# Optimization experiments

Hardware: AMD Instinct MI355X
Metric: run time of the kernel (lower is better)

Reference implementation:

```python
import jax, jax.numpy as jnp
import numpy as np

K = 31  # AvgPool2d kernel size
P = 15  # padding


def _box_avg(x):
    """31x31 stride-1 avg pool, count_include_pad=True (PyTorch default):
    separable ones-conv with zero padding, divided by K*K."""
    B, C, H, W = x.shape
    kh = jnp.ones((C, 1, K, 1), x.dtype)
    kw = jnp.ones((C, 1, 1, K), x.dtype)
    dn = ('NCHW', 'OIHW', 'NCHW')
    y = jax.lax.conv_general_dilated(x, kh, (1, 1), [(P, P), (0, 0)],
                                     dimension_numbers=dn, feature_group_count=C)
    y = jax.lax.conv_general_dilated(y, kw, (1, 1), [(0, 0), (P, P)],
                                     dimension_numbers=dn, feature_group_count=C)
    return y / (K * K)


def setup_inputs() -> dict:
    key = jax.random.key(0)
    k1, k2 = jax.random.split(key)
    pred = jax.random.normal(k1, (64, 1, 512, 512), dtype=jnp.float32)
    mask = jax.random.uniform(k2, (64, 1, 512, 512), dtype=jnp.float32)
    return {"pred": pred, "mask": mask}


def reference(pred, mask):
    weit = 1.0 + 5.0 * jnp.abs(_box_avg(mask) - mask)
    p = jax.nn.sigmoid(pred)
    inter = jnp.sum(p * mask * weit, axis=(2, 3))          # [B, C]
    union = jnp.sum((p + mask) * weit, axis=(2, 3))        # [B, C]
    wdiss = 1.0 - (2.0 * inter + 0.5) / (union + 0.5)
    return jnp.mean(wdiss)
```

## Files before the change

kernel.cpp:

```cpp
#include <hip/hip_runtime.h>
#include <math.h>

#define NB 64
#define HH 512
#define WW 512
#define KK 31
#define PP 15
#define TS 32
#define NSTRIP (HH / TS)
#define HR (TS + KK - 1)
#define NPAIR (HR / 2)

typedef _Float16 f16;
typedef f16 f16x8 __attribute__((ext_vector_type(8)));
typedef f16 f16x4 __attribute__((ext_vector_type(4)));
typedef f16 f16x2 __attribute__((ext_vector_type(2)));

__device__ __forceinline__ f16x2 shfl_up2(f16x2 v, int delta) {
    int x = __shfl_up(__builtin_bit_cast(int, v), delta);
    return __builtin_bit_cast(f16x2, x);
}
__device__ __forceinline__ f16x2 shfl_dn2(f16x2 v, int delta) {
    int x = __shfl_down(__builtin_bit_cast(int, v), delta);
    return __builtin_bit_cast(f16x2, x);
}
__device__ __forceinline__ f16x2 sel2(bool c, f16x2 v) {
    f16x2 z = {(f16)0, (f16)0};
    return c ? v : z;
}
__device__ __forceinline__ void keep4(float4& v) {
    asm volatile("" : "+v"(v.x), "+v"(v.y), "+v"(v.z), "+v"(v.w));
}


__global__ __launch_bounds__(512, 4) void dice_fused_kernel(
        const float* __restrict__ pred,
        const float* __restrict__ mask,
        float* __restrict__ part) {
    const int strip = blockIdx.x;
    const int b     = blockIdx.y;
    const int t     = threadIdx.x;
    const int wave  = t >> 6;
    const int lane  = t & 63;

    __shared__ f16 Hs[HR][WW];
    __shared__ float red[16];

    const float* mb = mask + (size_t)b * HH * WW;
    const float* pb = pred + (size_t)b * HH * WW;
    const int y0 = strip * TS;

    const int xbase = lane * 8;
    const bool lm1 = (lane >= 1);
    const bool lm2 = (lane >= 2);
    const bool lp1 = (lane <= 62);
    const bool lp2 = (lane <= 61);

    float va[4][8], vb[4][8];
    #pragma unroll
    for (int k = 0; k < 4; ++k) {
        const int p = k * 8 + wave;
        const int gya = y0 + 2 * p - PP;
        const int gyb = gya + 1;
        const bool pa = (p < NPAIR) && (gya >= 0) && (gya < HH);
        const bool qb = (p < NPAIR) && (gyb >= 0) && (gyb < HH);
        if (pa) {
            const float* row = mb + (size_t)gya * WW + xbase;
            const float4 u = *(const float4*)(row);
            const float4 v = *(const float4*)(row + 4);
            va[k][0] = u.x; va[k][1] = u.y; va[k][2] = u.z; va[k][3] = u.w;
            va[k][4] = v.x; va[k][5] = v.y; va[k][6] = v.z; va[k][7] = v.w;
        } else {
            #pragma unroll
            for (int j = 0; j < 8; ++j) va[k][j] = 0.0f;
        }
        if (qb) {
            const float* row = mb + (size_t)gyb * WW + xbase;
            const float4 u = *(const float4*)(row);
            const float4 v = *(const float4*)(row + 4);
            vb[k][0] = u.x; vb[k][1] = u.y; vb[k][2] = u.z; vb[k][3] = u.w;
            vb[k][4] = v.x; vb[k][5] = v.y; vb[k][6] = v.z; vb[k][7] = v.w;
        } else {
            #pragma unroll
            for (int j = 0; j < 8; ++j) vb[k][j] = 0.0f;
        }
    }

    #pragma unroll
    for (int k = 0; k < 4; ++k) {
        const int p = k * 8 + wave;
        if (p >= NPAIR) continue;
        const int ra = 2 * p;
        const int rb = ra + 1;

        float sa[8], sb[8];
        sa[0] = va[k][0]; sb[0] = vb[k][0];
        #pragma unroll
        for (int j = 1; j < 8; ++j) { sa[j] = sa[j-1] + va[k][j]; sb[j] = sb[j-1] + vb[k][j]; }

        f16x2 ps[8];
        #pragma unroll
        for (int j = 0; j < 8; ++j)
            ps[j] = __builtin_bit_cast(f16x2, __builtin_amdgcn_cvt_pkrtz(sa[j], sb[j]));
        const f16x2 pT = ps[7];

        f16x2 A[7];
        #pragma unroll
        for (int j = 0; j < 7; ++j) A[j] = shfl_up2(pT - ps[j], 2);
        const f16x2 Bprev = shfl_up2(pT, 1);
        const f16x2 Cfull = shfl_dn2(pT, 1);
        f16x2 Cp[7];
        #pragma unroll
        for (int j = 0; j < 7; ++j) Cp[j] = shfl_dn2(ps[j], 2);

        f16x2 base = pT;
        base += sel2(lm1, Bprev);
        base += sel2(lp1, Cfull);

        f16x8 ha, hb;
        #pragma unroll
        for (int j = 0; j < 8; ++j) {
            f16x2 acc = base;
            if (j < 7) acc += sel2(lm2, A[j]);
            if (j > 0) acc += sel2(lp2, Cp[j-1]);
            ha[j] = acc[0];
            hb[j] = acc[1];
        }
        *(f16x8*)&Hs[ra][xbase] = ha;
        *(f16x8*)&Hs[rb][xbase] = hb;
    }
    __syncthreads();

    const int q  = t & 127;
    const int g  = t >> 7;
    const int c  = q * 4;
    const int r0 = g * 8;

    float4 M[8], Pq[8];
    #pragma unroll
    for (int i = 0; i < 8; ++i) {
        const int y = y0 + r0 + i;
        M[i]  = *(const float4*)(mb + (size_t)y * WW + c);
        Pq[i] = *(const float4*)(pb + (size_t)y * WW + c);
    }
    #pragma unroll
    for (int i = 0; i < 8; ++i) { keep4(M[i]); keep4(Pq[i]); }

    f16x4 hl8[8], he8[8];
    f16x4 accA = {(f16)0, (f16)0, (f16)0, (f16)0};
    f16x4 accB = {(f16)0, (f16)0, (f16)0, (f16)0};
    #pragma unroll
    for (int j = 0; j < 8; ++j) {
        hl8[j] = *(const f16x4*)&Hs[r0 + j][c];
        accA += hl8[j];
    }
    #pragma unroll
    for (int j = 8; j < 15; ++j) accA += *(const f16x4*)&Hs[r0 + j][c];
    #pragma unroll
    for (int j = 15; j < 30; ++j) accB += *(const f16x4*)&Hs[r0 + j][c];
    #pragma unroll
    for (int i = 0; i < 8; ++i) he8[i] = *(const f16x4*)&Hs[r0 + 30 + i][c];

    float4 B;
    B.x = (float)accA[0] + (float)accB[0];
    B.y = (float)accA[1] + (float)accB[1];
    B.z = (float)accA[2] + (float)accB[2];
    B.w = (float)accA[3] + (float)accB[3];

    float4 I4 = make_float4(0.f, 0.f, 0.f, 0.f);
    float4 U4 = make_float4(0.f, 0.f, 0.f, 0.f);
    const float inv2 = 1.0f / (float)(KK * KK);

    #pragma unroll
    for (int i = 0; i < 8; ++i) {
        const f16x4 he = he8[i];
        const f16x4 hl = hl8[i];
        const float4 m4 = M[i];
        const float4 p4 = Pq[i];

        B.x += (float)he[0]; B.y += (float)he[1]; B.z += (float)he[2]; B.w += (float)he[3];

        const float w0 = fmaf(5.0f, fabsf(fmaf(B.x, inv2, -m4.x)), 1.0f);
        const float w1 = fmaf(5.0f, fabsf(fmaf(B.y, inv2, -m4.y)), 1.0f);
        const float w2 = fmaf(5.0f, fabsf(fmaf(B.z, inv2, -m4.z)), 1.0f);
        const float w3 = fmaf(5.0f, fabsf(fmaf(B.w, inv2, -m4.w)), 1.0f);
        const float sg0 = __builtin_amdgcn_rcpf(1.0f + __expf(-p4.x));
        const float sg1 = __builtin_amdgcn_rcpf(1.0f + __expf(-p4.y));
        const float sg2 = __builtin_amdgcn_rcpf(1.0f + __expf(-p4.z));
        const float sg3 = __builtin_amdgcn_rcpf(1.0f + __expf(-p4.w));

        I4.x = fmaf(sg0 * m4.x, w0, I4.x);  U4.x = fmaf(sg0 + m4.x, w0, U4.x);
        I4.y = fmaf(sg1 * m4.y, w1, I4.y);  U4.y = fmaf(sg1 + m4.y, w1, U4.y);
        I4.z = fmaf(sg2 * m4.z, w2, I4.z);  U4.z = fmaf(sg2 + m4.z, w2, U4.z);
        I4.w = fmaf(sg3 * m4.w, w3, I4.w);  U4.w = fmaf(sg3 + m4.w, w3, U4.w);

        B.x -= (float)hl[0]; B.y -= (float)hl[1]; B.z -= (float)hl[2]; B.w -= (float)hl[3];
    }

    float inter = I4.x + I4.y + I4.z + I4.w;
    float uni   = U4.x + U4.y + U4.z + U4.w;
    #pragma unroll
    for (int off = 32; off > 0; off >>= 1) {
        inter += __shfl_down(inter, off);
        uni   += __shfl_down(uni, off);
    }
    if (lane == 0) { red[wave] = inter; red[8 + wave] = uni; }
    __syncthreads();
    if (t == 0) {
        float ti = 0.f, tu = 0.f;
        #pragma unroll
        for (int w2 = 0; w2 < 8; ++w2) { ti += red[w2]; tu += red[8 + w2]; }
        const int bid = b * NSTRIP + strip;
        part[bid] = ti;
        part[NB * NSTRIP + bid] = tu;
    }
}

__global__ void dice_final_kernel(const float* __restrict__ part,
                                  float* __restrict__ out) {
    const int t = threadIdx.x;
    float inter = 0.0f, uni = 0.0f;
    #pragma unroll
    for (int s = 0; s < NSTRIP; ++s) {
        inter += part[t * NSTRIP + s];
        uni   += part[NB * NSTRIP + t * NSTRIP + s];
    }
    float wd = 1.0f - (2.0f * inter + 0.5f) / (uni + 0.5f);
    #pragma unroll
    for (int off = 32; off > 0; off >>= 1) wd += __shfl_down(wd, off);
    if (t == 0) out[0] = wd * (1.0f / (float)NB);
}

extern "C" void kernel_launch(void* const* d_in, const int* in_sizes, int n_in,
                              void* d_out, int out_size, void* d_ws, size_t ws_size,
                              hipStream_t stream) {
    const float* pred = (const float*)d_in[0];
    const float* mask = (const float*)d_in[1];
    float* out  = (float*)d_out;
    float* part = (float*)d_ws;

    dim3 grid(NSTRIP, NB);
    dice_fused_kernel<<<grid, 512, 0, stream>>>(pred, mask, part);
    dice_final_kernel<<<1, 64, 0, stream>>>(part, out);
}
```

Before: 150.2 us.

## Use taller strips with ring-buffered horizontal sums and cached fp16 mask rows

Each block now covers a 128-row strip instead of 32 rows. Horizontal box sums live in a 64-row LDS ring buffer that is refilled in chunks between vertical-pass phases, which cuts the 30-row halo re-reading from a ~2x overhead to ~1.23x. Mask rows for the block's own output are stored as fp16 in a second LDS ring, so the vertical pass no longer re-reads mask from global memory. In exchange, occupancy halves (launch bounds 2, double LDS), extra barriers are added, and the mask term in the weights is rounded to fp16.

```diff
diff --git a/kernel.cpp b/kernel.cpp
--- a/kernel.cpp
+++ b/kernel.cpp
@@ -6,10 +6,10 @@
 #define WW 512
 #define KK 31
 #define PP 15
-#define TS 32
-#define NSTRIP (HH / TS)
-#define HR (TS + KK - 1)
-#define NPAIR (HR / 2)
+#define TSP 128
+#define NSP (HH / TSP)
+#define RING 64
+#define RMASK (RING - 1)
 
 typedef _Float16 f16;
 typedef f16 f16x8 __attribute__((ext_vector_type(8)));
@@ -28,75 +28,67 @@
     f16x2 z = {(f16)0, (f16)0};
     return c ? v : z;
 }
-__device__ __forceinline__ void keep4(float4& v) {
-    asm volatile("" : "+v"(v.x), "+v"(v.y), "+v"(v.z), "+v"(v.w));
-}
-
-
-__global__ __launch_bounds__(512, 4) void dice_fused_kernel(
-        const float* __restrict__ pred,
-        const float* __restrict__ mask,
-        float* __restrict__ part) {
-    const int strip = blockIdx.x;
-    const int b     = blockIdx.y;
-    const int t     = threadIdx.x;
-    const int wave  = t >> 6;
-    const int lane  = t & 63;
-
-    __shared__ f16 Hs[HR][WW];
-    __shared__ float red[16];
-
-    const float* mb = mask + (size_t)b * HH * WW;
-    const float* pb = pred + (size_t)b * HH * WW;
-    const int y0 = strip * TS;
-
+
+template<int NK, bool CHECK>
+__device__ __forceinline__ void phase1_pairs(
+        const float* __restrict__ mb, f16 (* __restrict__ Hs)[WW],
+        f16 (* __restrict__ Ms)[WW],
+        const int y0, const int pfirst, const int wave, const int lane)
+{
     const int xbase = lane * 8;
     const bool lm1 = (lane >= 1);
     const bool lm2 = (lane >= 2);
     const bool lp1 = (lane <= 62);
     const bool lp2 = (lane <= 61);
 
-    float va[4][8], vb[4][8];
-    #pragma unroll
-    for (int k = 0; k < 4; ++k) {
-        const int p = k * 8 + wave;
-        const int gya = y0 + 2 * p - PP;
-        const int gyb = gya + 1;
-        const bool pa = (p < NPAIR) && (gya >= 0) && (gya < HH);
-        const bool qb = (p < NPAIR) && (gyb >= 0) && (gyb < HH);
-        if (pa) {
-            const float* row = mb + (size_t)gya * WW + xbase;
+    #pragma unroll
+    for (int k = 0; k < NK; ++k) {
+        const int p = pfirst + k * 8 + wave;
+        if (CHECK && p > 30) continue;
+        const int h0  = 2 * p;
+        const int gy0 = y0 + h0 - PP;
+        const int gy1 = gy0 + 1;
+
+        float va[8], vb[8];
+        if (gy0 >= 0 && gy0 < HH) {
+            const float* row = mb + (size_t)gy0 * WW + xbase;
             const float4 u = *(const float4*)(row);
             const float4 v = *(const float4*)(row + 4);
-            va[k][0] = u.x; va[k][1] = u.y; va[k][2] = u.z; va[k][3] = u.w;
-            va[k][4] = v.x; va[k][5] = v.y; va[k][6] = v.z; va[k][7] = v.w;
+            va[0] = u.x; va[1] = u.y; va[2] = u.z; va[3] = u.w;
+            va[4] = v.x; va[5] = v.y; va[6] = v.z; va[7] = v.w;
         } else {
             #pragma unroll
-            for (int j = 0; j < 8; ++j) va[k][j] = 0.0f;
-        }
-        if (qb) {
-            const float* row = mb + (size_t)gyb * WW + xbase;
+            for (int j = 0; j < 8; ++j) va[j] = 0.0f;
+        }
+        if (gy1 >= 0 && gy1 < HH) {
+            const float* row = mb + (size_t)gy1 * WW + xbase;
             const float4 u = *(const float4*)(row);
             const float4 v = *(const float4*)(row + 4);
-            vb[k][0] = u.x; vb[k][1] = u.y; vb[k][2] = u.z; vb[k][3] = u.w;
-            vb[k][4] = v.x; vb[k][5] = v.y; vb[k][6] = v.z; vb[k][7] = v.w;
+            vb[0] = u.x; vb[1] = u.y; vb[2] = u.z; vb[3] = u.w;
+            vb[4] = v.x; vb[5] = v.y; vb[6] = v.z; vb[7] = v.w;
         } else {
             #pragma unroll
-            for (int j = 0; j < 8; ++j) vb[k][j] = 0.0f;
-        }
-    }
-
-    #pragma unroll
-    for (int k = 0; k < 4; ++k) {
-        const int p = k * 8 + wave;
-        if (p >= NPAIR) continue;
-        const int ra = 2 * p;
-        const int rb = ra + 1;
+            for (int j = 0; j < 8; ++j) vb[j] = 0.0f;
+        }
+
+        const int yr0 = h0 - PP;
+        if (yr0 >= 0 && yr0 < TSP) {
+            f16x8 mv;
+            #pragma unroll
+            for (int j = 0; j < 8; ++j) mv[j] = (f16)va[j];
+            *(f16x8*)&Ms[yr0 & RMASK][xbase] = mv;
+        }
+        if (yr0 + 1 >= 0 && yr0 + 1 < TSP) {
+            f16x8 mv;
+            #pragma unroll
+            for (int j = 0; j < 8; ++j) mv[j] = (f16)vb[j];
+            *(f16x8*)&Ms[(yr0 + 1) & RMASK][xbase] = mv;
+        }
 
         float sa[8], sb[8];
-        sa[0] = va[k][0]; sb[0] = vb[k][0];
-        #pragma unroll
-        for (int j = 1; j < 8; ++j) { sa[j] = sa[j-1] + va[k][j]; sb[j] = sb[j-1] + vb[k][j]; }
+        sa[0] = va[0]; sb[0] = vb[0];
+        #pragma unroll
+        for (int j = 1; j < 8; ++j) { sa[j] = sa[j-1] + va[j]; sb[j] = sb[j-1] + vb[j]; }
 
         f16x2 ps[8];
         #pragma unroll
@@ -126,40 +118,31 @@
             ha[j] = acc[0];
             hb[j] = acc[1];
         }
-        *(f16x8*)&Hs[ra][xbase] = ha;
-        *(f16x8*)&Hs[rb][xbase] = hb;
-    }
-    __syncthreads();
-
-    const int q  = t & 127;
-    const int g  = t >> 7;
-    const int c  = q * 4;
-    const int r0 = g * 8;
-
-    float4 M[8], Pq[8];
-    #pragma unroll
-    for (int i = 0; i < 8; ++i) {
-        const int y = y0 + r0 + i;
-        M[i]  = *(const float4*)(mb + (size_t)y * WW + c);
-        Pq[i] = *(const float4*)(pb + (size_t)y * WW + c);
-    }
-    #pragma unroll
-    for (int i = 0; i < 8; ++i) { keep4(M[i]); keep4(Pq[i]); }
-
+        *(f16x8*)&Hs[h0 & RMASK][xbase] = ha;
+        *(f16x8*)&Hs[(h0 + 1) & RMASK][xbase] = hb;
+    }
+}
+
+__device__ __forceinline__ void phase2_half(
+        const float* __restrict__ pb,
+        const f16 (* __restrict__ Hs)[WW], const f16 (* __restrict__ Ms)[WW],
+        const int y0, const int r0h, const int c,
+        float4& I4, float4& U4)
+{
     f16x4 hl8[8], he8[8];
     f16x4 accA = {(f16)0, (f16)0, (f16)0, (f16)0};
     f16x4 accB = {(f16)0, (f16)0, (f16)0, (f16)0};
     #pragma unroll
     for (int j = 0; j < 8; ++j) {
-        hl8[j] = *(const f16x4*)&Hs[r0 + j][c];
+        hl8[j] = *(const f16x4*)&Hs[(r0h + j) & RMASK][c];
         accA += hl8[j];
     }
     #pragma unroll
-    for (int j = 8; j < 15; ++j) accA += *(const f16x4*)&Hs[r0 + j][c];
-    #pragma unroll
-    for (int j = 15; j < 30; ++j) accB += *(const f16x4*)&Hs[r0 + j][c];
-    #pragma unroll
-    for (int i = 0; i < 8; ++i) he8[i] = *(const f16x4*)&Hs[r0 + 30 + i][c];
+    for (int j = 8; j < 15; ++j) accA += *(const f16x4*)&Hs[(r0h + j) & RMASK][c];
+    #pragma unroll
+    for (int j = 15; j < 30; ++j) accB += *(const f16x4*)&Hs[(r0h + j) & RMASK][c];
+    #pragma unroll
+    for (int i = 0; i < 8; ++i) he8[i] = *(const f16x4*)&Hs[(r0h + 30 + i) & RMASK][c];
 
     float4 B;
     B.x = (float)accA[0] + (float)accB[0];
@@ -167,34 +150,75 @@
     B.z = (float)accA[2] + (float)accB[2];
     B.w = (float)accA[3] + (float)accB[3];
 
-    float4 I4 = make_float4(0.f, 0.f, 0.f, 0.f);
-    float4 U4 = make_float4(0.f, 0.f, 0.f, 0.f);
     const float inv2 = 1.0f / (float)(KK * KK);
 
     #pragma unroll
     for (int i = 0; i < 8; ++i) {
+        const int yr = r0h + i;
         const f16x4 he = he8[i];
         const f16x4 hl = hl8[i];
-        const float4 m4 = M[i];
-        const float4 p4 = Pq[i];
+        const f16x4 mm = *(const f16x4*)&Ms[yr & RMASK][c];
+        const float4 p4 = *(const float4*)(pb + (size_t)(y0 + yr) * WW + c);
+        const float m0 = (float)mm[0], m1 = (float)mm[1];
+        const float m2 = (float)mm[2], m3 = (float)mm[3];
 
         B.x += (float)he[0]; B.y += (float)he[1]; B.z += (float)he[2]; B.w += (float)he[3];
 
-        const float w0 = fmaf(5.0f, fabsf(fmaf(B.x, inv2, -m4.x)), 1.0f);
-        const float w1 = fmaf(5.0f, fabsf(fmaf(B.y, inv2, -m4.y)), 1.0f);
-        const float w2 = fmaf(5.0f, fabsf(fmaf(B.z, inv2, -m4.z)), 1.0f);
-        const float w3 = fmaf(5.0f, fabsf(fmaf(B.w, inv2, -m4.w)), 1.0f);
+        const float w0 = fmaf(5.0f, fabsf(fmaf(B.x, inv2, -m0)), 1.0f);
+        const float w1 = fmaf(5.0f, fabsf(fmaf(B.y, inv2, -m1)), 1.0f);
+        const float w2 = fmaf(5.0f, fabsf(fmaf(B.z, inv2, -m2)), 1.0f);
+        const float w3 = fmaf(5.0f, fabsf(fmaf(B.w, inv2, -m3)), 1.0f);
         const float sg0 = __builtin_amdgcn_rcpf(1.0f + __expf(-p4.x));
         const float sg1 = __builtin_amdgcn_rcpf(1.0f + __expf(-p4.y));
         const float sg2 = __builtin_amdgcn_rcpf(1.0f + __expf(-p4.z));
         const float sg3 = __builtin_amdgcn_rcpf(1.0f + __expf(-p4.w));
 
-        I4.x = fmaf(sg0 * m4.x, w0, I4.x);  U4.x = fmaf(sg0 + m4.x, w0, U4.x);
-        I4.y = fmaf(sg1 * m4.y, w1, I4.y);  U4.y = fmaf(sg1 + m4.y, w1, U4.y);
-        I4.z = fmaf(sg2 * m4.z, w2, I4.z);  U4.z = fmaf(sg2 + m4.z, w2, U4.z);
-        I4.w = fmaf(sg3 * m4.w, w3, I4.w);  U4.w = fmaf(sg3 + m4.w, w3, U4.w);
+        I4.x = fmaf(sg0 * m0, w0, I4.x);  U4.x = fmaf(sg0 + m0, w0, U4.x);
+        I4.y = fmaf(sg1 * m1, w1, I4.y);  U4.y = fmaf(sg1 + m1, w1, U4.y);
+        I4.z = fmaf(sg2 * m2, w2, I4.z);  U4.z = fmaf(sg2 + m2, w2, U4.z);
+        I4.w = fmaf(sg3 * m3, w3, I4.w);  U4.w = fmaf(sg3 + m3, w3, U4.w);
 
         B.x -= (float)hl[0]; B.y -= (float)hl[1]; B.z -= (float)hl[2]; B.w -= (float)hl[3];
+    }
+}
+
+
+__global__ __launch_bounds__(512, 2) void dice_fused_kernel(
+        const float* __restrict__ pred,
+        const float* __restrict__ mask,
+        float* __restrict__ part) {
+    const int sp = blockIdx.x;
+    const int b  = blockIdx.y;
+    const int t  = threadIdx.x;
+    const int wave = t >> 6;
+    const int lane = t & 63;
+
+    __shared__ f16 Hs[RING][WW];
+    __shared__ f16 Ms[RING][WW];
+    __shared__ float red[16];
+
+    const float* mb = mask + (size_t)b * HH * WW;
+    const float* pb = pred + (size_t)b * HH * WW;
+    const int y0 = sp * TSP;
+
+    phase1_pairs<4, true>(mb, Hs, Ms, y0, 0, wave, lane);
+    __syncthreads();
+
+    const int q = t & 127;
+    const int g = t >> 7;
+    const int c = q * 4;
+
+    float4 I4 = make_float4(0.f, 0.f, 0.f, 0.f);
+    float4 U4 = make_float4(0.f, 0.f, 0.f, 0.f);
+
+    #pragma unroll
+    for (int half = 0; half < 4; ++half) {
+        phase2_half(pb, Hs, Ms, y0, g * 8 + 32 * half, c, I4, U4);
+        __syncthreads();
+        if (half < 3) {
+            phase1_pairs<2, false>(mb, Hs, Ms, y0, 31 + 16 * half, wave, lane);
+            __syncthreads();
+        }
     }
 
     float inter = I4.x + I4.y + I4.z + I4.w;
@@ -210,9 +234,9 @@
         float ti = 0.f, tu = 0.f;
         #pragma unroll
         for (int w2 = 0; w2 < 8; ++w2) { ti += red[w2]; tu += red[8 + w2]; }
-        const int bid = b * NSTRIP + strip;
+        const int bid = b * NSP + sp;
         part[bid] = ti;
-        part[NB * NSTRIP + bid] = tu;
+        part[NB * NSP + bid] = tu;
     }
 }
 
@@ -221,9 +245,9 @@
     const int t = threadIdx.x;
     float inter = 0.0f, uni = 0.0f;
     #pragma unroll
-    for (int s = 0; s < NSTRIP; ++s) {
-        inter += part[t * NSTRIP + s];
-        uni   += part[NB * NSTRIP + t * NSTRIP + s];
+    for (int s = 0; s < NSP; ++s) {
+        inter += part[t * NSP + s];
+        uni   += part[NB * NSP + t * NSP + s];
     }
     float wd = 1.0f - (2.0f * inter + 0.5f) / (uni + 0.5f);
     #pragma unroll
@@ -239,7 +263,7 @@
     float* out  = (float*)d_out;
     float* part = (float*)d_ws;
 
-    dim3 grid(NSTRIP, NB);
+    dim3 grid(NSP, NB);
     dice_fused_kernel<<<grid, 512, 0, stream>>>(pred, mask, part);
     dice_final_kernel<<<1, 64, 0, stream>>>(part, out);
 }
```

Measured after the change: 146.4 us. 1.03x faster.
